# Optimization experiments

Measured on AMD Instinct MI355X. Metric: run time of the kernel, lower is better.

The kernel has to match this reference:

```python
import jax, jax.numpy as jnp
import numpy as np

N_NODES = 100000
N_EDGES = 1600000
D_FEAT = 128
HIDDEN = 128
HEADS = 4
OUT_C = HIDDEN // HEADS  # 32
N_CLASSES = 10
N_GRAPHS = 64
NEG_SLOPE = 0.2


def glorot(key, shape, fan_in, fan_out):
    s = jnp.sqrt(6.0 / (fan_in + fan_out))
    return jax.random.uniform(key, shape, minval=-s, maxval=s, dtype=jnp.float32)


def setup_inputs() -> dict:
    key = jax.random.key(0)
    ks = jax.random.split(key, 24)
    x = jax.random.normal(ks[0], (N_NODES, D_FEAT), dtype=jnp.float32)
    src = jax.random.randint(ks[1], (N_EDGES,), 0, N_NODES, dtype=jnp.int32)
    off = jax.random.randint(ks[2], (N_EDGES,), 1, N_NODES, dtype=jnp.int32)
    dst = ((src + off) % N_NODES).astype(jnp.int32)  # guarantees no self-loops
    edge_index = jnp.stack([src, dst], axis=0)
    batch = jnp.sort(jax.random.randint(ks[3], (N_NODES,), 0, N_GRAPHS, dtype=jnp.int32))
    inp = {"x": x, "edge_index": edge_index, "batch": batch}
    # GATConv layer params: W [in, H*C] (lin_l == lin_r), att_l/att_r [H, C], bias [H*C]
    ins = [D_FEAT, HIDDEN, HIDDEN]
    for i in range(3):
        k = 4 + 4 * i
        inp[f"W{i+1}"] = glorot(ks[k], (ins[i], HEADS * OUT_C), ins[i], HEADS * OUT_C)
        inp[f"al{i+1}"] = glorot(ks[k + 1], (HEADS, OUT_C), HEADS * OUT_C, 1)
        inp[f"ar{i+1}"] = glorot(ks[k + 2], (HEADS, OUT_C), HEADS * OUT_C, 1)
        inp[f"b{i+1}"] = jnp.zeros((HEADS * OUT_C,), jnp.float32)
    inp["lin1_w"] = glorot(ks[16], (HIDDEN, HIDDEN), HIDDEN, HIDDEN)
    inp["lin1_b"] = jnp.zeros((HIDDEN,), jnp.float32)
    inp["lin2_w"] = glorot(ks[17], (HIDDEN, N_CLASSES), HIDDEN, N_CLASSES)
    inp["lin2_b"] = jnp.zeros((N_CLASSES,), jnp.float32)
    return inp


def gat_layer(x, src, dst, W, att_l, att_r, bias):
    n = x.shape[0]
    H, C = att_l.shape
    xw = (x @ W).reshape(n, H, C)                       # Theta x
    al = jnp.einsum('nhc,hc->nh', xw, att_l)
    ar = jnp.einsum('nhc,hc->nh', xw, att_r)
    loop = jnp.arange(n, dtype=src.dtype)
    s = jnp.concatenate([src, loop])                    # add self-loops
    d = jnp.concatenate([dst, loop])
    logits = jax.nn.leaky_relu(al[s] + ar[d], NEG_SLOPE)  # [E+N, H]
    m = jax.ops.segment_max(logits, d, num_segments=n)    # segment softmax over dst
    e = jnp.exp(logits - m[d])
    z = jax.ops.segment_sum(e, d, num_segments=n)
    alpha = e / z[d]
    msg = xw[s] * alpha[:, :, None]                     # [E+N, H, C]
    out = jax.ops.segment_sum(msg, d, num_segments=n)   # scatter-add aggregate
    return out.reshape(n, H * C) + bias


def reference(x, edge_index, batch,
              W1, al1, ar1, b1, W2, al2, ar2, b2, W3, al3, ar3, b3,
              lin1_w, lin1_b, lin2_w, lin2_b):
    src, dst = edge_index[0], edge_index[1]
    h = jax.nn.relu(gat_layer(x, src, dst, W1, al1, ar1, b1))
    h = jax.nn.relu(gat_layer(h, src, dst, W2, al2, ar2, b2))
    h = jax.nn.relu(gat_layer(h, src, dst, W3, al3, ar3, b3))
    last = h
    # global mean pool over graphs in the batch
    s = jax.ops.segment_sum(h, batch, num_segments=N_GRAPHS)
    cnt = jax.ops.segment_sum(jnp.ones((h.shape[0],), h.dtype), batch, num_segments=N_GRAPHS)
    pooled = s / jnp.maximum(cnt, 1.0)[:, None]
    g = jax.nn.relu(pooled @ lin1_w + lin1_b)           # dropout inactive (eval)
    logits = g @ lin2_w + lin2_b
    return (jax.nn.log_softmax(logits, axis=-1), last)
```

## Files before the change

kernel.cpp:

```cpp
#include <hip/hip_runtime.h>
#include <math.h>


#define LRELU(x) ((x) > 0.f ? (x) : 0.2f*(x))
#define SH 8
#define TILE 4096
#define EPT 16

typedef __attribute__((ext_vector_type(8))) short s16x8;
typedef __attribute__((ext_vector_type(4))) float f32x4;

__device__ inline unsigned short f2bf(float f){
  unsigned u = __float_as_uint(f);
  u += 0x7fff + ((u >> 16) & 1);
  return (unsigned short)(u >> 16);
}

__global__ void k_init(int* __restrict__ bcnt, float* __restrict__ psum){
  int t = threadIdx.x;
  bcnt[t] = 0; bcnt[256 + t] = 0;
  for (int i = t; i < 8192; i += 256) psum[i] = 0.f;
}

template<bool BF16IN>
__device__ __forceinline__ void gemm_body(
    unsigned short* Wt, unsigned short* Xl,
    const void* __restrict__ Xv, const float* __restrict__ W,
    const float* __restrict__ attl, const float* __restrict__ attr,
    unsigned short* __restrict__ XW, float* __restrict__ AL, float* __restrict__ AR,
    int n, int bid, int gstride)
{
  int t = threadIdx.x;
  int lane = t & 63, w = t >> 6;
  int l15 = lane & 15, quad = lane >> 4;
  for (int i = 0; i < 64; i++){
    int e = i*256 + t;
    int k = e >> 7, nn = e & 127;
    Wt[nn*128 + ((((k>>3) ^ (nn&15))<<3) | (k&7))] = f2bf(W[e]);
  }
  int ntiles = (n + 63) >> 6;
  int r_ = t >> 2, seg = t & 3;
  for (int tile = bid; tile < ntiles; tile += gstride){
    int row0 = tile << 6;
    __syncthreads();
    {
      int grow = row0 + r_;
      unsigned short* dp = &Xl[r_*136 + seg*32];
      if (grow < n){
        if (BF16IN){
          const uint4* gp = (const uint4*)((const unsigned short*)Xv + (size_t)grow*128 + seg*32);
          #pragma unroll
          for (int i = 0; i < 4; i++) ((uint4*)dp)[i] = gp[i];
        } else {
          const float4* gp = (const float4*)((const float*)Xv + (size_t)grow*128 + seg*32);
          #pragma unroll
          for (int i = 0; i < 8; i++){
            float4 v = gp[i];
            ((unsigned*)dp)[i*2]   = (unsigned)f2bf(v.x) | ((unsigned)f2bf(v.y) << 16);
            ((unsigned*)dp)[i*2+1] = (unsigned)f2bf(v.z) | ((unsigned)f2bf(v.w) << 16);
          }
        }
      } else {
        #pragma unroll
        for (int i = 0; i < 4; i++) ((uint4*)dp)[i] = make_uint4(0,0,0,0);
      }
    }
    __syncthreads();
    f32x4 acc[4][2];
    #pragma unroll
    for (int rt = 0; rt < 4; rt++){ acc[rt][0] = (f32x4){0,0,0,0}; acc[rt][1] = (f32x4){0,0,0,0}; }
    #pragma unroll
    for (int ks = 0; ks < 4; ks++){
      s16x8 b0 = *(const s16x8*)&Wt[(w*32 + l15)*128      + (((ks*4+quad) ^ l15)<<3)];
      s16x8 b1 = *(const s16x8*)&Wt[(w*32 + 16 + l15)*128 + (((ks*4+quad) ^ l15)<<3)];
      #pragma unroll
      for (int rt = 0; rt < 4; rt++){
        s16x8 a = *(const s16x8*)&Xl[(rt*16 + l15)*136 + ks*32 + quad*8];
        acc[rt][0] = __builtin_amdgcn_mfma_f32_16x16x32_bf16(a, b0, acc[rt][0], 0, 0, 0);
        acc[rt][1] = __builtin_amdgcn_mfma_f32_16x16x32_bf16(a, b1, acc[rt][1], 0, 0, 0);
      }
    }
    __syncthreads();
    #pragma unroll
    for (int rt = 0; rt < 4; rt++)
      #pragma unroll
      for (int c2 = 0; c2 < 2; c2++)
        #pragma unroll
        for (int r = 0; r < 4; r++)
          Xl[(rt*16 + quad*4 + r)*136 + w*32 + c2*16 + l15] = f2bf(acc[rt][c2][r]);
    __syncthreads();
    {
      int grow = row0 + r_;
      if (grow < n){
        const unsigned short* sp = &Xl[r_*136 + seg*32];
        uint4 uu[4];
        #pragma unroll
        for (int i = 0; i < 4; i++) uu[i] = ((const uint4*)sp)[i];
        unsigned short* gx = XW + (size_t)grow*128 + seg*32;
        #pragma unroll
        for (int i = 0; i < 4; i++) ((uint4*)gx)[i] = uu[i];
        const unsigned* up = (const unsigned*)uu;
        const float4* alp = (const float4*)(attl + seg*32);
        const float4* arp = (const float4*)(attr + seg*32);
        float pl = 0.f, pr = 0.f;
        #pragma unroll
        for (int i = 0; i < 8; i++){
          unsigned ua = up[i*2], ub = up[i*2+1];
          float x0 = __uint_as_float(ua << 16);
          float x1 = __uint_as_float(ua & 0xffff0000u);
          float x2 = __uint_as_float(ub << 16);
          float x3 = __uint_as_float(ub & 0xffff0000u);
          float4 av = alp[i];
          float4 rv = arp[i];
          pl += x0*av.x + x1*av.y + x2*av.z + x3*av.w;
          pr += x0*rv.x + x1*rv.y + x2*rv.z + x3*rv.w;
        }
        AL[grow*4 + seg] = pl;
        AR[grow*4 + seg] = pr;
      }
    }
  }
}

template<bool BF16IN>
__global__ __launch_bounds__(256) void k_gemm(
    const void* __restrict__ Xv, const float* __restrict__ W,
    const float* __restrict__ attl, const float* __restrict__ attr,
    unsigned short* __restrict__ XW, float* __restrict__ AL, float* __restrict__ AR, int n)
{
  __shared__ unsigned short Wt[128*128];
  __shared__ unsigned short Xl[64*136];
  gemm_body<BF16IN>(Wt, Xl, Xv, W, attl, attr, XW, AL, AR, n, blockIdx.x, gridDim.x);
}

__global__ __launch_bounds__(256) void k_fuse1(
    const int* __restrict__ dst, int* __restrict__ bcnt, int E, int nparts,
    const float* __restrict__ X, const float* __restrict__ W,
    const float* __restrict__ attl, const float* __restrict__ attr,
    unsigned short* __restrict__ XW, float* __restrict__ AL, float* __restrict__ AR, int n)
{
  __shared__ unsigned short Wt[128*128];
  __shared__ unsigned short Xl[64*136];
  if ((int)blockIdx.x < nparts){
    int* lh = (int*)Wt;
    int t = threadIdx.x;
    for (int j = t; j < 512; j += 256) lh[j] = 0;
    __syncthreads();
    int base = blockIdx.x * TILE;
    int lim = min(base + TILE, E);
    for (int e = base + t; e < lim; e += 256)
      atomicAdd(&lh[dst[e] >> SH], 1);
    __syncthreads();
    for (int j = t; j < 512; j += 256){
      int v = lh[j];
      if (v) atomicAdd(&bcnt[j], v);
    }
    return;
  }
  gemm_body<false>(Wt, Xl, X, W, attl, attr, XW, AL, AR, n,
                   (int)blockIdx.x - nparts, (int)gridDim.x - nparts);
}

__global__ __launch_bounds__(256) void k_bscan(const int* __restrict__ bcnt,
    int* __restrict__ bstart, int* __restrict__ bfill, int NB, int E,
    const int* __restrict__ batch, int* __restrict__ gstart, int n){
  int t = threadIdx.x;
  if (blockIdx.x == 1){
    int g = t;
    if (g > 64) return;
    int lo = 0, hi = n;
    while (lo < hi){
      int mid = (lo + hi) >> 1;
      if (batch[mid] < g) lo = mid + 1; else hi = mid;
    }
    gstart[g] = lo;
    return;
  }
  __shared__ int c[512];
  __shared__ int ps[256];
  for (int j = t; j < 512; j += 256) c[j] = (j < NB) ? bcnt[j] : 0;
  __syncthreads();
  int b0 = 2*t;
  int v0 = c[b0], v1 = c[b0+1];
  int ts = v0 + v1;
  ps[t] = ts; __syncthreads();
  for (int off = 1; off < 256; off <<= 1){
    int x = (t >= off) ? ps[t-off] : 0; __syncthreads();
    ps[t] += x; __syncthreads();
  }
  int pre = ps[t] - ts;
  if (b0   < NB){ bstart[b0]   = pre;    bfill[b0]   = pre; }
  if (b0+1 < NB){ bstart[b0+1] = pre+v0; bfill[b0+1] = pre+v0; }
  if (t == 0) bstart[NB] = E;
}

__global__ __launch_bounds__(256) void k_part(const int* __restrict__ src,
    const int* __restrict__ dst, int* __restrict__ bfill,
    int2* __restrict__ tmp, int E){
  __shared__ int2 reorder[TILE];
  __shared__ int lhist[512], lscan[512], lgbase[512];
  __shared__ int ps[256];
  int t = threadIdx.x;
  int tb = blockIdx.x * TILE;
  int tilecnt = min(TILE, E - tb);
  for (int j = t; j < 512; j += 256) lhist[j] = 0;
  __syncthreads();
  int ss[EPT], dd[EPT], rk[EPT];
  #pragma unroll
  for (int i = 0; i < EPT; i++){
    int e = tb + t + i*256;
    if (e < E){
      ss[i] = src[e]; dd[i] = dst[e];
      rk[i] = atomicAdd(&lhist[dd[i] >> SH], 1);
    }
  }
  __syncthreads();
  int b0 = 2*t;
  int v0 = lhist[b0], v1 = lhist[b0+1];
  int ts = v0 + v1;
  ps[t] = ts; __syncthreads();
  for (int off = 1; off < 256; off <<= 1){
    int x = (t >= off) ? ps[t-off] : 0; __syncthreads();
    ps[t] += x; __syncthreads();
  }
  int pre = ps[t] - ts;
  int ex0 = pre, ex1 = pre + v0;
  lscan[b0] = ex0; lscan[b0+1] = ex1;
  if (v0 > 0){ int gb = atomicAdd(&bfill[b0],   v0); lgbase[b0]   = gb - ex0; }
  if (v1 > 0){ int gb = atomicAdd(&bfill[b0+1], v1); lgbase[b0+1] = gb - ex1; }
  __syncthreads();
  #pragma unroll
  for (int i = 0; i < EPT; i++){
    int e = tb + t + i*256;
    if (e < E){
      int b = dd[i] >> SH;
      reorder[lscan[b] + rk[i]] = make_int2(ss[i], dd[i]);
    }
  }
  __syncthreads();
  for (int j = t; j < tilecnt; j += 256){
    int2 p = reorder[j];
    tmp[lgbase[p.y >> SH] + j] = p;
  }
}

__global__ __launch_bounds__(256) void k_csr(const int2* __restrict__ tmp,
    const int* __restrict__ bstart, int* __restrict__ rp, int* __restrict__ col,
    int n, int E){
  __shared__ int lcnt[256];
  __shared__ int sc[256];
  int b = blockIdx.x, t = threadIdx.x;
  int node0 = b << SH;
  int ncnt = min(256, n - node0);
  int be = bstart[b], ee = bstart[b+1];
  lcnt[t] = 0;
  __syncthreads();
  for (int e = be + t; e < ee; e += 256)
    atomicAdd(&lcnt[tmp[e].y - node0], 1);
  __syncthreads();
  int v = lcnt[t];
  sc[t] = v;
  __syncthreads();
  for (int off = 1; off < 256; off <<= 1){
    int x = (t >= off) ? sc[t-off] : 0;
    __syncthreads();
    sc[t] += x;
    __syncthreads();
  }
  int start = be + sc[t] - v;
  lcnt[t] = start;
  if (t < ncnt) rp[node0 + t] = start;
  if (t == 0 && node0 + ncnt == n) rp[n] = E;
  __syncthreads();
  for (int e = be + t; e < ee; e += 256){
    int2 p = tmp[e];
    int pos = atomicAdd(&lcnt[p.y - node0], 1);
    col[pos] = p.x;
  }
}

template<bool BF16OUT>
__global__ __launch_bounds__(256) void k_attn(
    const unsigned short* __restrict__ XW, const float* __restrict__ AL, const float* __restrict__ AR,
    const int* __restrict__ rp, const int* __restrict__ col,
    const float* __restrict__ bias, void* __restrict__ OUT, int n)
{
  __shared__ float ebuf[4][68*4];
  __shared__ int   sbuf[4][68];
  int wv = threadIdx.x >> 6;
  int d = blockIdx.x*4 + wv;
  int lane = threadIdx.x & 63;
  if (d >= n) return;
  float* eb = ebuf[wv];
  int*   sb = sbuf[wv];
  if (lane < 16) eb[256 + lane] = 0.f;
  if (lane < 4)  sb[64 + lane] = 0;
  int start = rp[d], end = rp[d+1];
  float4 ald4 = ((const float4*)AL)[d];
  float4 ard4 = ((const float4*)AR)[d];
  float ar0 = ard4.x, ar1 = ard4.y, ar2 = ard4.z, ar3 = ard4.w;
  float es0 = __expf(LRELU(ald4.x + ar0));
  float es1 = __expf(LRELU(ald4.y + ar1));
  float es2 = __expf(LRELU(ald4.z + ar2));
  float es3 = __expf(LRELU(ald4.w + ar3));
  int r   = lane & 15;
  int row = lane >> 4;
  int h2  = r >> 2;
  float eself = h2==0?es0 : h2==1?es1 : h2==2?es2 : es3;
  const uint4* XW4 = (const uint4*)XW;
  float acc[8];
  {
    uint4 v = XW4[(unsigned)d*16 + r];
    float sw = (row == 0) ? eself : 0.f;
    acc[0] = sw * __uint_as_float(v.x << 16);
    acc[1] = sw * __uint_as_float(v.x & 0xffff0000u);
    acc[2] = sw * __uint_as_float(v.y << 16);
    acc[3] = sw * __uint_as_float(v.y & 0xffff0000u);
    acc[4] = sw * __uint_as_float(v.z << 16);
    acc[5] = sw * __uint_as_float(v.z & 0xffff0000u);
    acc[6] = sw * __uint_as_float(v.w << 16);
    acc[7] = sw * __uint_as_float(v.w & 0xffff0000u);
  }
  float zl0 = 0.f, zl1 = 0.f, zl2 = 0.f, zl3 = 0.f;
  for (int base = start; base < end; base += 64){
    int cnt = min(64, end - base);
    int s = (lane < cnt) ? col[base + lane] : 0;
    float4 a = ((const float4*)AL)[s];
    float w0 = __expf(LRELU(a.x + ar0));
    float w1 = __expf(LRELU(a.y + ar1));
    float w2 = __expf(LRELU(a.z + ar2));
    float w3 = __expf(LRELU(a.w + ar3));
    if (lane >= cnt){ w0 = w1 = w2 = w3 = 0.f; }
    zl0 += w0; zl1 += w1; zl2 += w2; zl3 += w3;
    float4 w4; w4.x = w0; w4.y = w1; w4.z = w2; w4.w = w3;
    ((float4*)eb)[lane] = w4;
    sb[lane] = s << 4;
    #pragma unroll 4
    for (int j = 0; j < cnt; j += 4){
      int jr = j + row;
      int sj = sb[jr] + r;
      float w = eb[jr*4 + h2];
      uint4 u = XW4[sj];
      acc[0] = fmaf(w, __uint_as_float(u.x << 16), acc[0]);
      acc[1] = fmaf(w, __uint_as_float(u.x & 0xffff0000u), acc[1]);
      acc[2] = fmaf(w, __uint_as_float(u.y << 16), acc[2]);
      acc[3] = fmaf(w, __uint_as_float(u.y & 0xffff0000u), acc[3]);
      acc[4] = fmaf(w, __uint_as_float(u.z << 16), acc[4]);
      acc[5] = fmaf(w, __uint_as_float(u.z & 0xffff0000u), acc[5]);
      acc[6] = fmaf(w, __uint_as_float(u.w << 16), acc[6]);
      acc[7] = fmaf(w, __uint_as_float(u.w & 0xffff0000u), acc[7]);
    }
  }
  #pragma unroll
  for (int off = 32; off >= 1; off >>= 1){
    zl0 += __shfl_xor(zl0, off, 64);
    zl1 += __shfl_xor(zl1, off, 64);
    zl2 += __shfl_xor(zl2, off, 64);
    zl3 += __shfl_xor(zl3, off, 64);
  }
  #pragma unroll
  for (int i = 0; i < 8; i++){
    acc[i] += __shfl_xor(acc[i], 16, 64);
    acc[i] += __shfl_xor(acc[i], 32, 64);
  }
  float z_h = (h2==0?zl0 : h2==1?zl1 : h2==2?zl2 : zl3) + eself;
  float rz = 1.f / z_h;
  float4 b0 = ((const float4*)bias)[r*2];
  float4 b1 = ((const float4*)bias)[r*2 + 1];
  float o[8];
  o[0] = fmaf(acc[0], rz, b0.x); o[1] = fmaf(acc[1], rz, b0.y);
  o[2] = fmaf(acc[2], rz, b0.z); o[3] = fmaf(acc[3], rz, b0.w);
  o[4] = fmaf(acc[4], rz, b1.x); o[5] = fmaf(acc[5], rz, b1.y);
  o[6] = fmaf(acc[6], rz, b1.z); o[7] = fmaf(acc[7], rz, b1.w);
  #pragma unroll
  for (int i = 0; i < 8; i++) o[i] = o[i] > 0.f ? o[i] : 0.f;
  if (row == 0){
    if (BF16OUT){
      uint4 pk;
      pk.x = (unsigned)f2bf(o[0]) | ((unsigned)f2bf(o[1]) << 16);
      pk.y = (unsigned)f2bf(o[2]) | ((unsigned)f2bf(o[3]) << 16);
      pk.z = (unsigned)f2bf(o[4]) | ((unsigned)f2bf(o[5]) << 16);
      pk.w = (unsigned)f2bf(o[6]) | ((unsigned)f2bf(o[7]) << 16);
      ((uint4*)OUT)[(unsigned)d*16 + r] = pk;
    } else {
      float4 f0; f0.x = o[0]; f0.y = o[1]; f0.z = o[2]; f0.w = o[3];
      float4 f1; f1.x = o[4]; f1.y = o[5]; f1.z = o[6]; f1.w = o[7];
      ((float4*)OUT)[(unsigned)d*32 + r*2]     = f0;
      ((float4*)OUT)[(unsigned)d*32 + r*2 + 1] = f1;
    }
  }
}

__global__ __launch_bounds__(128) void k_pool(const float* __restrict__ H,
                                              const int* __restrict__ gstart,
                                              float* __restrict__ psum){
  int g = blockIdx.x >> 3, slice = blockIdx.x & 7, t = threadIdx.x;
  int s0 = gstart[g], s1 = gstart[g+1];
  int cntg = s1 - s0;
  int chunk = (cntg + 7) >> 3;
  int lo = s0 + slice*chunk;
  int hi = min(lo + chunk, s1);
  float sum = 0.f;
  for (int i = lo; i < hi; i++) sum += H[(size_t)i*128 + t];
  atomicAdd(&psum[g*128 + t], sum);
}

__global__ __launch_bounds__(128) void k_mlp(const float* __restrict__ psum,
                       const int* __restrict__ gstart,
                       const float* __restrict__ w1, const float* __restrict__ b1,
                       const float* __restrict__ w2, const float* __restrict__ b2,
                       float* __restrict__ out)
{
  __shared__ float p[128];
  __shared__ float gsh[128];
  __shared__ float lg[10];
  int g = blockIdx.x, t = threadIdx.x;
  float c = fmaxf((float)(gstart[g+1] - gstart[g]), 1.f);
  p[t] = psum[g*128 + t] / c;
  __syncthreads();
  float acc = b1[t];
  for (int k = 0; k < 128; k++) acc = fmaf(p[k], w1[k*128 + t], acc);
  gsh[t] = acc > 0.f ? acc : 0.f;
  __syncthreads();
  if (t < 10){
    float a = b2[t];
    for (int k = 0; k < 128; k++) a = fmaf(gsh[k], w2[k*10 + t], a);
    lg[t] = a;
  }
  __syncthreads();
  if (t < 10){
    float mx = lg[0];
    for (int c2 = 1; c2 < 10; c2++) mx = fmaxf(mx, lg[c2]);
    float se = 0.f;
    for (int c2 = 0; c2 < 10; c2++) se += __expf(lg[c2] - mx);
    out[g*10 + t] = lg[t] - mx - logf(se);
  }
}

extern "C" void kernel_launch(void* const* d_in, const int* in_sizes, int n_in,
                              void* d_out, int out_size, void* d_ws, size_t ws_size,
                              hipStream_t stream)
{
  const float* x    = (const float*)d_in[0];
  const int* eidx   = (const int*)d_in[1];
  const int* batch  = (const int*)d_in[2];
  const float* W[3]  = {(const float*)d_in[3], (const float*)d_in[7],  (const float*)d_in[11]};
  const float* al[3] = {(const float*)d_in[4], (const float*)d_in[8],  (const float*)d_in[12]};
  const float* ar[3] = {(const float*)d_in[5], (const float*)d_in[9],  (const float*)d_in[13]};
  const float* bs[3] = {(const float*)d_in[6], (const float*)d_in[10], (const float*)d_in[14]};
  const float* l1w = (const float*)d_in[15];
  const float* l1b = (const float*)d_in[16];
  const float* l2w = (const float*)d_in[17];
  const float* l2b = (const float*)d_in[18];
  int E = in_sizes[1] / 2;
  int n = in_sizes[2];
  const int* srcp = eidx;
  const int* dstp = eidx + E;
  int NB = (n + 255) >> SH;

  char* wsp = (char*)d_ws;
  auto alloc = [&](size_t bytes){ void* p = (void*)wsp; wsp += (bytes + 255) & ~(size_t)255; return p; };
  unsigned short* xw   = (unsigned short*)alloc((size_t)n*128*2);
  unsigned short* hbuf = (unsigned short*)alloc((size_t)n*128*2);
  float* ALb  = (float*)alloc((size_t)n*4*4);
  float* ARb  = (float*)alloc((size_t)n*4*4);
  int* rp     = (int*)alloc((size_t)(n+1)*4);
  int* col    = (int*)alloc((size_t)E*4);
  int2* tmp   = (int2*)alloc((size_t)E*8);
  int* bcnt   = (int*)alloc(512*4);
  int* bstart = (int*)alloc(513*4);
  int* bfill  = (int*)alloc(512*4);
  float* psum = (float*)alloc(64*128*4);
  int* gstart = (int*)alloc(65*4);

  float* outlog = (float*)d_out;
  float* h3     = (float*)d_out + 64*10;

  int nparts = (E + TILE - 1) / TILE;

  k_init<<<1, 256, 0, stream>>>(bcnt, psum);
  k_fuse1<<<nparts + 768, 256, 0, stream>>>(dstp, bcnt, E, nparts,
                                            x, W[0], al[0], ar[0], xw, ALb, ARb, n);
  k_bscan<<<2, 256, 0, stream>>>(bcnt, bstart, bfill, NB, E, batch, gstart, n);
  k_part <<<nparts, 256, 0, stream>>>(srcp, dstp, bfill, tmp, E);
  k_csr  <<<NB, 256, 0, stream>>>(tmp, bstart, rp, col, n, E);

  k_attn<true><<<(n+3)/4, 256, 0, stream>>>(xw, ALb, ARb, rp, col, bs[0], hbuf, n);
  k_gemm<true><<<768, 256, 0, stream>>>(hbuf, W[1], al[1], ar[1], xw, ALb, ARb, n);
  k_attn<true><<<(n+3)/4, 256, 0, stream>>>(xw, ALb, ARb, rp, col, bs[1], hbuf, n);
  k_gemm<true><<<768, 256, 0, stream>>>(hbuf, W[2], al[2], ar[2], xw, ALb, ARb, n);
  k_attn<false><<<(n+3)/4, 256, 0, stream>>>(xw, ALb, ARb, rp, col, bs[2], h3, n);

  k_pool<<<64*8, 128, 0, stream>>>(h3, gstart, psum);
  k_mlp <<<64, 128, 0, stream>>>(psum, gstart, l1w, l1b, l2w, l2b, outlog);
}
```

Measured before the change: 593.1 us.

## Process four destination nodes per wavefront in GAT attention kernel

Measured after the change: 570.0 us. 1.04x faster.

```diff
diff --git a/kernel.cpp b/kernel.cpp
--- a/kernel.cpp
+++ b/kernel.cpp
@@ -285,62 +285,70 @@
     const int* __restrict__ rp, const int* __restrict__ col,
     const float* __restrict__ bias, void* __restrict__ OUT, int n)
 {
-  __shared__ float ebuf[4][68*4];
-  __shared__ int   sbuf[4][68];
+  __shared__ int   ws[4][512];
+  __shared__ float arsh[4][4][4];
   int wv = threadIdx.x >> 6;
-  int d = blockIdx.x*4 + wv;
   int lane = threadIdx.x & 63;
-  if (d >= n) return;
-  float* eb = ebuf[wv];
-  int*   sb = sbuf[wv];
-  if (lane < 16) eb[256 + lane] = 0.f;
-  if (lane < 4)  sb[64 + lane] = 0;
-  int start = rp[d], end = rp[d+1];
-  float4 ald4 = ((const float4*)AL)[d];
-  float4 ard4 = ((const float4*)AR)[d];
-  float ar0 = ard4.x, ar1 = ard4.y, ar2 = ard4.z, ar3 = ard4.w;
-  float es0 = __expf(LRELU(ald4.x + ar0));
-  float es1 = __expf(LRELU(ald4.y + ar1));
-  float es2 = __expf(LRELU(ald4.z + ar2));
-  float es3 = __expf(LRELU(ald4.w + ar3));
-  int r   = lane & 15;
-  int row = lane >> 4;
-  int h2  = r >> 2;
-  float eself = h2==0?es0 : h2==1?es1 : h2==2?es2 : es3;
+  int r = lane & 15, g = lane >> 4, h2 = r >> 2;
+  int d0 = (blockIdx.x*4 + wv)*4;
+  if (d0 >= n) return;
+  int d = d0 + g;
+  bool valid = d < n;
+  int dc = valid ? d : n-1;
+  int rs = rp[dc];
+  int re = valid ? rp[dc+1] : rs;
+  float4 ard4 = ((const float4*)AR)[dc];
+  if (r == 0) *(float4*)&arsh[wv][g][0] = ard4;
+  float4 ald4 = ((const float4*)AL)[dc];
+  float alh = h2==0?ald4.x : h2==1?ald4.y : h2==2?ald4.z : ald4.w;
+  float arh = h2==0?ard4.x : h2==1?ard4.y : h2==2?ard4.z : ard4.w;
+  float tse = alh + arh;
+  float eself = __expf(fmaxf(tse, 0.2f*tse));
   const uint4* XW4 = (const uint4*)XW;
+  float zacc = eself;
   float acc[8];
   {
-    uint4 v = XW4[(unsigned)d*16 + r];
-    float sw = (row == 0) ? eself : 0.f;
-    acc[0] = sw * __uint_as_float(v.x << 16);
-    acc[1] = sw * __uint_as_float(v.x & 0xffff0000u);
-    acc[2] = sw * __uint_as_float(v.y << 16);
-    acc[3] = sw * __uint_as_float(v.y & 0xffff0000u);
-    acc[4] = sw * __uint_as_float(v.z << 16);
-    acc[5] = sw * __uint_as_float(v.z & 0xffff0000u);
-    acc[6] = sw * __uint_as_float(v.w << 16);
-    acc[7] = sw * __uint_as_float(v.w & 0xffff0000u);
-  }
-  float zl0 = 0.f, zl1 = 0.f, zl2 = 0.f, zl3 = 0.f;
-  for (int base = start; base < end; base += 64){
-    int cnt = min(64, end - base);
-    int s = (lane < cnt) ? col[base + lane] : 0;
-    float4 a = ((const float4*)AL)[s];
-    float w0 = __expf(LRELU(a.x + ar0));
-    float w1 = __expf(LRELU(a.y + ar1));
-    float w2 = __expf(LRELU(a.z + ar2));
-    float w3 = __expf(LRELU(a.w + ar3));
-    if (lane >= cnt){ w0 = w1 = w2 = w3 = 0.f; }
-    zl0 += w0; zl1 += w1; zl2 += w2; zl3 += w3;
-    float4 w4; w4.x = w0; w4.y = w1; w4.z = w2; w4.w = w3;
-    ((float4*)eb)[lane] = w4;
-    sb[lane] = s << 4;
+    uint4 v = XW4[(size_t)dc*16 + r];
+    acc[0] = eself * __uint_as_float(v.x << 16);
+    acc[1] = eself * __uint_as_float(v.x & 0xffff0000u);
+    acc[2] = eself * __uint_as_float(v.y << 16);
+    acc[3] = eself * __uint_as_float(v.y & 0xffff0000u);
+    acc[4] = eself * __uint_as_float(v.z << 16);
+    acc[5] = eself * __uint_as_float(v.z & 0xffff0000u);
+    acc[6] = eself * __uint_as_float(v.w << 16);
+    acc[7] = eself * __uint_as_float(v.w & 0xffff0000u);
+  }
+  int ub0 = rp[d0];
+  int ubE = rp[min(d0+4, n)];
+  int reb = valid ? re : 0x7fffffff;
+  int b1 = __shfl(reb, 0, 64);
+  int b2 = __shfl(reb, 16, 64);
+  int b3 = __shfl(reb, 32, 64);
+  int* wsw = ws[wv];
+  for (int cb = ub0; cb < ubE; cb += 64){
+    int cnt = min(64, ubE - cb);
+    if (lane < cnt){
+      int e = cb + lane;
+      int s = col[e];
+      int eg = (e >= b1) + (e >= b2) + (e >= b3);
+      float4 arr = *(const float4*)&arsh[wv][eg][0];
+      float4 a = ((const float4*)AL)[s];
+      float t0 = a.x + arr.x, t1 = a.y + arr.y, t2 = a.z + arr.z, t3 = a.w + arr.w;
+      float w0 = __expf(fmaxf(t0, 0.2f*t0));
+      float w1 = __expf(fmaxf(t1, 0.2f*t1));
+      float w2 = __expf(fmaxf(t2, 0.2f*t2));
+      float w3 = __expf(fmaxf(t3, 0.2f*t3));
+      int s4 = s << 4;
+      ((int4*)&wsw[lane*8])[0] = make_int4(s4, __float_as_int(w0), s4, __float_as_int(w1));
+      ((int4*)&wsw[lane*8])[1] = make_int4(s4, __float_as_int(w2), s4, __float_as_int(w3));
+    }
+    int jlo = max(rs - cb, 0);
+    int jhi = min(re - cb, cnt);
     #pragma unroll 4
-    for (int j = 0; j < cnt; j += 4){
-      int jr = j + row;
-      int sj = sb[jr] + r;
-      float w = eb[jr*4 + h2];
-      uint4 u = XW4[sj];
+    for (int j = jlo; j < jhi; ++j){
+      int2 q = *(const int2*)&wsw[j*8 + h2*2];
+      float w = __int_as_float(q.y);
+      uint4 u = XW4[(unsigned)(q.x + r)];
       acc[0] = fmaf(w, __uint_as_float(u.x << 16), acc[0]);
       acc[1] = fmaf(w, __uint_as_float(u.x & 0xffff0000u), acc[1]);
       acc[2] = fmaf(w, __uint_as_float(u.y << 16), acc[2]);
@@ -349,44 +357,32 @@
       acc[5] = fmaf(w, __uint_as_float(u.z & 0xffff0000u), acc[5]);
       acc[6] = fmaf(w, __uint_as_float(u.w << 16), acc[6]);
       acc[7] = fmaf(w, __uint_as_float(u.w & 0xffff0000u), acc[7]);
-    }
-  }
-  #pragma unroll
-  for (int off = 32; off >= 1; off >>= 1){
-    zl0 += __shfl_xor(zl0, off, 64);
-    zl1 += __shfl_xor(zl1, off, 64);
-    zl2 += __shfl_xor(zl2, off, 64);
-    zl3 += __shfl_xor(zl3, off, 64);
-  }
-  #pragma unroll
-  for (int i = 0; i < 8; i++){
-    acc[i] += __shfl_xor(acc[i], 16, 64);
-    acc[i] += __shfl_xor(acc[i], 32, 64);
-  }
-  float z_h = (h2==0?zl0 : h2==1?zl1 : h2==2?zl2 : zl3) + eself;
-  float rz = 1.f / z_h;
-  float4 b0 = ((const float4*)bias)[r*2];
-  float4 b1 = ((const float4*)bias)[r*2 + 1];
+      zacc += w;
+    }
+  }
+  float rz = 1.f / zacc;
+  float4 bb0 = ((const float4*)bias)[r*2];
+  float4 bb1 = ((const float4*)bias)[r*2 + 1];
   float o[8];
-  o[0] = fmaf(acc[0], rz, b0.x); o[1] = fmaf(acc[1], rz, b0.y);
-  o[2] = fmaf(acc[2], rz, b0.z); o[3] = fmaf(acc[3], rz, b0.w);
-  o[4] = fmaf(acc[4], rz, b1.x); o[5] = fmaf(acc[5], rz, b1.y);
-  o[6] = fmaf(acc[6], rz, b1.z); o[7] = fmaf(acc[7], rz, b1.w);
+  o[0] = fmaf(acc[0], rz, bb0.x); o[1] = fmaf(acc[1], rz, bb0.y);
+  o[2] = fmaf(acc[2], rz, bb0.z); o[3] = fmaf(acc[3], rz, bb0.w);
+  o[4] = fmaf(acc[4], rz, bb1.x); o[5] = fmaf(acc[5], rz, bb1.y);
+  o[6] = fmaf(acc[6], rz, bb1.z); o[7] = fmaf(acc[7], rz, bb1.w);
   #pragma unroll
   for (int i = 0; i < 8; i++) o[i] = o[i] > 0.f ? o[i] : 0.f;
-  if (row == 0){
+  if (valid){
     if (BF16OUT){
       uint4 pk;
       pk.x = (unsigned)f2bf(o[0]) | ((unsigned)f2bf(o[1]) << 16);
       pk.y = (unsigned)f2bf(o[2]) | ((unsigned)f2bf(o[3]) << 16);
       pk.z = (unsigned)f2bf(o[4]) | ((unsigned)f2bf(o[5]) << 16);
       pk.w = (unsigned)f2bf(o[6]) | ((unsigned)f2bf(o[7]) << 16);
-      ((uint4*)OUT)[(unsigned)d*16 + r] = pk;
+      ((uint4*)OUT)[(size_t)d*16 + r] = pk;
     } else {
       float4 f0; f0.x = o[0]; f0.y = o[1]; f0.z = o[2]; f0.w = o[3];
       float4 f1; f1.x = o[4]; f1.y = o[5]; f1.z = o[6]; f1.w = o[7];
-      ((float4*)OUT)[(unsigned)d*32 + r*2]     = f0;
-      ((float4*)OUT)[(unsigned)d*32 + r*2 + 1] = f1;
+      ((float4*)OUT)[(size_t)d*32 + r*2]     = f0;
+      ((float4*)OUT)[(size_t)d*32 + r*2 + 1] = f1;
     }
   }
 }
@@ -485,11 +481,12 @@
   k_part <<<nparts, 256, 0, stream>>>(srcp, dstp, bfill, tmp, E);
   k_csr  <<<NB, 256, 0, stream>>>(tmp, bstart, rp, col, n, E);
 
-  k_attn<true><<<(n+3)/4, 256, 0, stream>>>(xw, ALb, ARb, rp, col, bs[0], hbuf, n);
+  int ablk = (n + 15) / 16;
+  k_attn<true><<<ablk, 256, 0, stream>>>(xw, ALb, ARb, rp, col, bs[0], hbuf, n);
   k_gemm<true><<<768, 256, 0, stream>>>(hbuf, W[1], al[1], ar[1], xw, ALb, ARb, n);
-  k_attn<true><<<(n+3)/4, 256, 0, stream>>>(xw, ALb, ARb, rp, col, bs[1], hbuf, n);
+  k_attn<true><<<ablk, 256, 0, stream>>>(xw, ALb, ARb, rp, col, bs[1], hbuf, n);
   k_gemm<true><<<768, 256, 0, stream>>>(hbuf, W[2], al[2], ar[2], xw, ALb, ARb, n);
-  k_attn<false><<<(n+3)/4, 256, 0, stream>>>(xw, ALb, ARb, rp, col, bs[2], h3, n);
+  k_attn<false><<<ablk, 256, 0, stream>>>(xw, ALb, ARb, rp, col, bs[2], h3, n);
 
   k_pool<<<64*8, 128, 0, stream>>>(h3, gstart, psum);
   k_mlp <<<64, 128, 0, stream>>>(psum, gstart, l1w, l1b, l2w, l2b, outlog);
```
